# Kernel optimization log

Measured on AMD Instinct MI355X. Metric: run time of the kernel, lower is better.

## Reference

```python
import jax, jax.numpy as jnp
import numpy as np

DIM = 2048
HEADS = 16
HEAD_DIM = DIM // HEADS
EPS = 1e-5


def layernorm(x, g, b):
    mu = jnp.mean(x, axis=-1, keepdims=True)
    var = jnp.mean(jnp.square(x - mu), axis=-1, keepdims=True)
    return (x - mu) * jax.lax.rsqrt(var + EPS) * g + b


def bitlinear(x, w):
    # BitNet b1.58: per-tensor ternary weight quant + per-token int8 absmax activation quant
    ws = jnp.clip(jnp.mean(jnp.abs(w)), 1e-5, None)          # weight scale (mean |w|)
    wq = jnp.clip(jnp.round(w / ws), -1.0, 1.0) * ws          # ternary {-1,0,1}*ws
    xs = 127.0 / jnp.clip(jnp.max(jnp.abs(x), axis=-1, keepdims=True), 1e-5, None)
    xq = jnp.clip(jnp.round(x * xs), -128.0, 127.0) / xs      # int8 absmax, dequantized
    return jnp.einsum('bnc,oc->bno', xq, wq)


def attention(x, w_qkv, w_proj):
    B, N, C = x.shape
    qkv = bitlinear(x, w_qkv).reshape(B, N, 3, HEADS, HEAD_DIM)
    q, k, v = [qkv[:, :, i].transpose(0, 2, 1, 3) for i in range(3)]  # [B,H,N,D]
    scores = jnp.einsum('bhqd,bhkd->bhqk', q, k) / jnp.sqrt(jnp.asarray(HEAD_DIM, x.dtype))
    attn = jax.nn.softmax(scores, axis=-1)
    o = jnp.einsum('bhqk,bhkd->bhqd', attn, v)
    o = o.transpose(0, 2, 1, 3).reshape(B, N, C)
    return bitlinear(o, w_proj)


def setup_inputs() -> dict:
    key = jax.random.key(0)
    ks = jax.random.split(key, 9)
    s = 0.02
    return {
        'x': jax.random.normal(ks[0], (2, 2048, DIM), dtype=jnp.float32),
        'w_qkv': jax.random.normal(ks[1], (3 * DIM, DIM), dtype=jnp.float32) * s,
        'w_proj': jax.random.normal(ks[2], (DIM, DIM), dtype=jnp.float32) * s,
        'w_fc1': jax.random.normal(ks[3], (4 * DIM, DIM), dtype=jnp.float32) * s,
        'w_fc2': jax.random.normal(ks[4], (DIM, 4 * DIM), dtype=jnp.float32) * s,
        'g1': jnp.ones((DIM,), jnp.float32),
        'b1': jnp.zeros((DIM,), jnp.float32),
        'g2': jnp.ones((DIM,), jnp.float32),
        'b2': jnp.zeros((DIM,), jnp.float32),
    }


def reference(x, w_qkv, w_proj, w_fc1, w_fc2, g1, b1, g2, b2):
    x = x + attention(layernorm(x, g1, b1), w_qkv, w_proj)
    h = bitlinear(layernorm(x, g2, b2), w_fc1)
    h = jax.nn.gelu(h, approximate=False)
    h = bitlinear(h, w_fc2)
    return x + h
```

## Files before the change

### kernel.cpp

```cpp
#include <hip/hip_runtime.h>
#include <cstdint>

#define DEVI __device__ __forceinline__

typedef int v4i __attribute__((ext_vector_type(4)));
typedef short v8s __attribute__((ext_vector_type(8)));
typedef float v4f __attribute__((ext_vector_type(4)));

DEVI float bf_lo(unsigned u) { return __uint_as_float(u << 16); }
DEVI float bf_hi(unsigned u) { return __uint_as_float(u & 0xffff0000u); }
DEVI float bf2f(unsigned short h) { return __uint_as_float(((unsigned)h) << 16); }
DEVI unsigned short f2bf(float f) {
  unsigned u = __float_as_uint(f);
  u += 0x7fffu + ((u >> 16) & 1u);
  return (unsigned short)(u >> 16);
}

DEVI void async_copy16(void* l, const void* g) {
  __builtin_amdgcn_global_load_lds((const __attribute__((address_space(1))) void*)g,
                                   (__attribute__((address_space(3))) void*)l,
                                   16, 0, 0);
}

DEVI float wave_sum(float v) {
#pragma unroll
  for (int o = 32; o > 0; o >>= 1) v += __shfl_xor(v, o, 64);
  return v;
}
DEVI float wave_max(float v) {
#pragma unroll
  for (int o = 32; o > 0; o >>= 1) v = fmaxf(v, __shfl_xor(v, o, 64));
  return v;
}

__global__ __launch_bounds__(256) void absum_kernel(const float* __restrict__ w, long n,
                                                    float* __restrict__ acc) {
  long stride = (long)gridDim.x * 1024;
  float s = 0.f;
  for (long i = ((long)blockIdx.x * 256 + threadIdx.x) * 4; i < n; i += stride) {
    float4 v = *(const float4*)(w + i);
    s += fabsf(v.x) + fabsf(v.y) + fabsf(v.z) + fabsf(v.w);
  }
  s = wave_sum(s);
  __shared__ float sc[4];
  int tid = threadIdx.x;
  if ((tid & 63) == 0) sc[tid >> 6] = s;
  __syncthreads();
  if (tid == 0) atomicAdd(acc, sc[0] + sc[1] + sc[2] + sc[3]);
}

__global__ __launch_bounds__(256) void wquant_kernel(const float* __restrict__ w, long n4,
                                                     const float* __restrict__ acc, float cnt,
                                                     signed char* __restrict__ out, int kshift) {
  float wsv = fmaxf(acc[0] / cnt, 1e-5f);
  float inv = 1.0f / wsv;
  int K = 1 << kshift;
  long stride = (long)gridDim.x * 256;
  for (long i = (long)blockIdx.x * 256 + threadIdx.x; i < n4; i += stride) {
    float4 v = *(const float4*)(w + i * 4);
    int q0 = max(-1, min(1, (int)rintf(v.x * inv)));
    int q1 = max(-1, min(1, (int)rintf(v.y * inv)));
    int q2 = max(-1, min(1, (int)rintf(v.z * inv)));
    int q3 = max(-1, min(1, (int)rintf(v.w * inv)));
    unsigned r = (q0 & 0xff) | ((q1 & 0xff) << 8) | ((q2 & 0xff) << 16) | ((q3 & 0xff) << 24);
    long flat = i * 4;
    int n = (int)(flat >> kshift);
    int k = (int)(flat & (K - 1));
    long off = ((long)(n >> 4) * (K >> 6) + (k >> 6)) * 1024 +
               (((k >> 4) & 3) * 16 + (n & 15)) * 16 + (k & 15);
    *(unsigned*)(out + off) = r;
  }
}

__global__ __launch_bounds__(256) void ln_quant_kernel(const float* __restrict__ x,
                                                       const float* __restrict__ g,
                                                       const float* __restrict__ b,
                                                       signed char* __restrict__ q,
                                                       float* __restrict__ inv_s) {
  int row = blockIdx.x, tid = threadIdx.x;
  const float4* xr = (const float4*)(x + (long)row * 2048);
  float4 a0 = xr[tid * 2], a1 = xr[tid * 2 + 1];
  float xv[8] = {a0.x, a0.y, a0.z, a0.w, a1.x, a1.y, a1.z, a1.w};
  float s = 0.f, s2 = 0.f;
#pragma unroll
  for (int e = 0; e < 8; ++e) { s += xv[e]; s2 += xv[e] * xv[e]; }
  s = wave_sum(s); s2 = wave_sum(s2);
  __shared__ float sc[8];
  if ((tid & 63) == 0) { sc[tid >> 6] = s; sc[4 + (tid >> 6)] = s2; }
  __syncthreads();
  float mean = (sc[0] + sc[1] + sc[2] + sc[3]) * (1.f / 2048.f);
  float var = (sc[4] + sc[5] + sc[6] + sc[7]) * (1.f / 2048.f) - mean * mean;
  float rs = 1.0f / sqrtf(var + 1e-5f);
  float4 g0 = ((const float4*)g)[tid * 2], g1v = ((const float4*)g)[tid * 2 + 1];
  float4 b0 = ((const float4*)b)[tid * 2], b1v = ((const float4*)b)[tid * 2 + 1];
  float gv[8] = {g0.x, g0.y, g0.z, g0.w, g1v.x, g1v.y, g1v.z, g1v.w};
  float bv[8] = {b0.x, b0.y, b0.z, b0.w, b1v.x, b1v.y, b1v.z, b1v.w};
  float y[8];
  float am = 0.f;
#pragma unroll
  for (int e = 0; e < 8; ++e) {
    y[e] = (xv[e] - mean) * rs * gv[e] + bv[e];
    am = fmaxf(am, fabsf(y[e]));
  }
  am = wave_max(am);
  __syncthreads();
  if ((tid & 63) == 0) sc[tid >> 6] = am;
  __syncthreads();
  am = fmaxf(fmaxf(sc[0], sc[1]), fmaxf(sc[2], sc[3]));
  float c = fmaxf(am, 1e-5f);
  float xs = 127.0f / c;
  union { signed char c8[8]; int2 v; } u;
#pragma unroll
  for (int e = 0; e < 8; ++e) {
    int t = (int)rintf(y[e] * xs);
    u.c8[e] = (signed char)max(-128, min(127, t));
  }
  ((int2*)(q + (long)row * 2048))[tid] = u.v;
  if (tid == 0) inv_s[row] = c * (1.0f / 127.0f);
}

template <int R>
__global__ __launch_bounds__(256) void row_quant_kernel(const unsigned short* __restrict__ in,
                                                        signed char* __restrict__ q,
                                                        float* __restrict__ inv_s) {
  constexpr int V = R / 2048;
  int row = blockIdx.x, tid = threadIdx.x;
  const uint4* p = (const uint4*)(in + (long)row * R);
  float y[V * 8];
  float am = 0.f;
#pragma unroll
  for (int v = 0; v < V; ++v) {
    uint4 d = p[tid * V + v];
    unsigned xw[4] = {d.x, d.y, d.z, d.w};
#pragma unroll
    for (int k = 0; k < 4; ++k) {
      y[v * 8 + k * 2] = bf_lo(xw[k]);
      y[v * 8 + k * 2 + 1] = bf_hi(xw[k]);
    }
  }
#pragma unroll
  for (int e = 0; e < V * 8; ++e) am = fmaxf(am, fabsf(y[e]));
  am = wave_max(am);
  __shared__ float sc[4];
  if ((tid & 63) == 0) sc[tid >> 6] = am;
  __syncthreads();
  am = fmaxf(fmaxf(sc[0], sc[1]), fmaxf(sc[2], sc[3]));
  float c = fmaxf(am, 1e-5f);
  float xs = 127.0f / c;
  signed char* qr = q + (long)row * R;
#pragma unroll
  for (int v = 0; v < V; ++v) {
    union { signed char c8[8]; long l; } u;
#pragma unroll
    for (int k = 0; k < 8; ++k) {
      int t = (int)rintf(y[v * 8 + k] * xs);
      u.c8[k] = (signed char)max(-128, min(127, t));
    }
    ((long*)qr)[tid * V + v] = u.l;
  }
  if (tid == 0) inv_s[row] = c * (1.0f / 127.0f);
}

template <int EPI>
__global__ __launch_bounds__(256)
void gemm_i8(const signed char* __restrict__ A, const signed char* __restrict__ Bp,
             int N, int K, const float* __restrict__ wacc, float wcount,
             const float* __restrict__ inv_s, const float* __restrict__ res,
             void* __restrict__ outp) {
  __shared__ signed char As[2][128 * 128];
  int tid = threadIdx.x;
  int idx = blockIdx.x;
  int r8 = idx & 7, rest = idx >> 3;
  int mb = rest & 31;
  int nb = (rest >> 5) * 8 + r8;
  int m0 = mb * 128, n0 = nb * 128;
  int w = tid >> 6, lane = tid & 63;
  int wm = (w >> 1) * 64, wn = (w & 1) * 64;
  int lr = lane & 15, q = lane >> 4;

  v4i acc[4][4] = {};

  int srow = w * 32 + (lane >> 3);
  int scol = (lane & 7) ^ ((lane >> 3) & 7);
  const signed char* ga = A + (long)(m0 + srow) * K + scol * 16;

  int nkb = K >> 7;
  const signed char* gbp[4];
#pragma unroll
  for (int t = 0; t < 4; ++t) {
    int ntile = (n0 >> 4) + (w & 1) * 4 + t;
    gbp[t] = Bp + (long)ntile * (K >> 6) * 1024 + lane * 16;
  }

  v4i bf_cur[2][4], bf_nxt[2][4];
#pragma unroll
  for (int i = 0; i < 4; ++i)
    async_copy16(&As[0][(w * 256 + i * 64) * 16], ga + i * 8 * K);
#pragma unroll
  for (int s = 0; s < 2; ++s)
#pragma unroll
    for (int t = 0; t < 4; ++t) bf_cur[s][t] = *(const v4i*)(gbp[t] + s * 1024);
  __syncthreads();

  int buf = 0;
  for (int kb = 0; kb < nkb; ++kb) {
    if (kb + 1 < nkb) {
#pragma unroll
      for (int i = 0; i < 4; ++i)
        async_copy16(&As[buf ^ 1][(w * 256 + i * 64) * 16], ga + i * 8 * K + (kb + 1) * 128);
#pragma unroll
      for (int s = 0; s < 2; ++s)
#pragma unroll
        for (int t = 0; t < 4; ++t)
          bf_nxt[s][t] = *(const v4i*)(gbp[t] + ((kb + 1) * 2 + s) * 1024);
    }
#pragma unroll
    for (int s = 0; s < 2; ++s) {
      v4i af[4];
#pragma unroll
      for (int i = 0; i < 4; ++i) {
        int row = wm + i * 16 + lr;
        af[i] = *(const v4i*)(&As[buf][(row * 8 + ((s * 4 + q) ^ (lr & 7))) * 16]);
      }
#pragma unroll
      for (int i = 0; i < 4; ++i)
#pragma unroll
        for (int j = 0; j < 4; ++j)
          acc[i][j] = __builtin_amdgcn_mfma_i32_16x16x64_i8(af[i], bf_cur[s][j], acc[i][j], 0, 0, 0);
    }
    __syncthreads();
    if (kb + 1 < nkb) {
#pragma unroll
      for (int s = 0; s < 2; ++s)
#pragma unroll
        for (int t = 0; t < 4; ++t) bf_cur[s][t] = bf_nxt[s][t];
    }
    buf ^= 1;
  }

  float wsv = fmaxf(wacc[0] / wcount, 1e-5f);
#pragma unroll
  for (int i = 0; i < 4; ++i) {
    int rowbase = m0 + wm + i * 16 + (lane >> 4) * 4;
#pragma unroll
    for (int r = 0; r < 4; ++r) {
      int row = rowbase + r;
      float s = wsv * inv_s[row];
#pragma unroll
      for (int j = 0; j < 4; ++j) {
        int col = n0 + wn + j * 16 + (lane & 15);
        long off = (long)row * N + col;
        float v = (float)acc[i][j][r] * s;
        if constexpr (EPI == 0) {
          ((unsigned short*)outp)[off] = f2bf(v);
        } else if constexpr (EPI == 1) {
          ((float*)outp)[off] = v + res[off];
        } else {
          float gvv = 0.5f * v * (1.0f + erff(v * 0.70710678118654752f));
          ((unsigned short*)outp)[off] = f2bf(gvv);
        }
      }
    }
  }
}

__global__ __launch_bounds__(256, 2)
void fattn_kernel(const unsigned short* __restrict__ qkv, float* __restrict__ O0,
                  float* __restrict__ O1, float2* __restrict__ stats) {
  constexpr int VROW = 72;
  constexpr int PROW = 72;
  __shared__ char Ks[16384];
  __shared__ unsigned short Vt[128 * VROW];
  __shared__ unsigned short Ps[4 * 32 * PROW];

  int tid = threadIdx.x;
  int w = tid >> 6, lane = tid & 63;
  int l = lane & 15, q = lane >> 4;
  int idx = blockIdx.x;
  int r8 = idx & 7, rest = idx >> 3;
  int ks = rest & 1;
  int qt = (rest >> 1) & 15;
  int bh = (rest >> 5) * 8 + r8;
  int bb = bh >> 4, hh = bh & 15;
  const unsigned short* base = qkv + (long)bb * 2048 * 6144;
  int q0 = qt * 128;
  float* Opart = ks ? O1 : O0;

  v8s aq[2][4];
#pragma unroll
  for (int s = 0; s < 2; ++s) {
    const unsigned short* qrow = base + (long)(q0 + w * 32 + s * 16 + l) * 6144 + hh * 128;
#pragma unroll
    for (int kf = 0; kf < 4; ++kf) aq[s][kf] = *(const v8s*)(qrow + kf * 32 + q * 8);
  }

  v4f oacc[2][8];
#pragma unroll
  for (int s = 0; s < 2; ++s)
#pragma unroll
    for (int t = 0; t < 8; ++t) oacc[s][t] = (v4f){0.f, 0.f, 0.f, 0.f};
  float mrow[2][4], lrow[2][4];
#pragma unroll
  for (int s = 0; s < 2; ++s)
#pragma unroll
    for (int r = 0; r < 4; ++r) { mrow[s][r] = -1e30f; lrow[s][r] = 0.f; }

  unsigned short* pw = Ps + w * 32 * PROW;
  const unsigned short* kbase_g = base + 2048 + hh * 128;
  const unsigned short* vbase_g = base + 4096 + hh * 128;
  int kg = tid & 7, dg = tid >> 3;
  constexpr float SC = 0.08838834764831845f;

  for (int kt = ks * 16; kt < ks * 16 + 16; ++kt) {
    int k0 = kt * 64;
#pragma unroll
    for (int i = 0; i < 4; ++i) {
      int c = i * 256 + w * 64 + lane;
      int key = c >> 4;
      int dch = (c & 15) ^ (key & 15);
      async_copy16(Ks + (i * 256 + w * 64) * 16,
                   kbase_g + (long)(k0 + key) * 6144 + dch * 8);
    }
    {
      uint2 lv[8];
#pragma unroll
      for (int i = 0; i < 8; ++i)
        lv[i] = *(const uint2*)(vbase_g + (long)(k0 + kg * 8 + i) * 6144 + dg * 4);
#pragma unroll
      for (int jd = 0; jd < 4; ++jd) {
        v8s pk;
#pragma unroll
        for (int i = 0; i < 8; ++i) {
          unsigned word = (jd < 2) ? lv[i].x : lv[i].y;
          pk[i] = (short)((jd & 1) ? (word >> 16) : (word & 0xffffu));
        }
        *(v8s*)(Vt + (dg * 4 + jd) * VROW + kg * 8) = pk;
      }
    }
    __syncthreads();

    v4f sacc[2][4];
#pragma unroll
    for (int s = 0; s < 2; ++s)
#pragma unroll
      for (int t = 0; t < 4; ++t) sacc[s][t] = (v4f){0.f, 0.f, 0.f, 0.f};
#pragma unroll
    for (int kf = 0; kf < 4; ++kf) {
#pragma unroll
      for (int t = 0; t < 4; ++t) {
        int ch = (t * 16 + l) * 16 + ((kf * 4 + q) ^ l);
        v8s bk = *(const v8s*)(Ks + ch * 16);
        sacc[0][t] = __builtin_amdgcn_mfma_f32_16x16x32_bf16(aq[0][kf], bk, sacc[0][t], 0, 0, 0);
        sacc[1][t] = __builtin_amdgcn_mfma_f32_16x16x32_bf16(aq[1][kf], bk, sacc[1][t], 0, 0, 0);
      }
    }
#pragma unroll
    for (int s = 0; s < 2; ++s) {
      float rmax[4], alpha[4], rsum[4];
#pragma unroll
      for (int r = 0; r < 4; ++r) {
        rmax[r] = fmaxf(fmaxf(sacc[s][0][r], sacc[s][1][r]),
                        fmaxf(sacc[s][2][r], sacc[s][3][r])) * SC;
#pragma unroll
        for (int msk = 1; msk < 16; msk <<= 1) rmax[r] = fmaxf(rmax[r], __shfl_xor(rmax[r], msk, 64));
        float mnew = fmaxf(mrow[s][r], rmax[r]);
        alpha[r] = __expf(mrow[s][r] - mnew);
        mrow[s][r] = mnew;
        rsum[r] = 0.f;
      }
#pragma unroll
      for (int t = 0; t < 4; ++t) {
#pragma unroll
        for (int r = 0; r < 4; ++r) {
          float p = __expf(sacc[s][t][r] * SC - mrow[s][r]);
          rsum[r] += p;
          pw[(s * 16 + q * 4 + r) * PROW + t * 16 + l] = f2bf(p);
        }
      }
#pragma unroll
      for (int r = 0; r < 4; ++r) {
#pragma unroll
        for (int msk = 1; msk < 16; msk <<= 1) rsum[r] += __shfl_xor(rsum[r], msk, 64);
        lrow[s][r] = lrow[s][r] * alpha[r] + rsum[r];
#pragma unroll
        for (int t = 0; t < 8; ++t) oacc[s][t][r] *= alpha[r];
      }
    }
#pragma unroll
    for (int s2 = 0; s2 < 2; ++s2) {
      v8s ap0 = *(const v8s*)(pw + l * PROW + s2 * 32 + q * 8);
      v8s ap1 = *(const v8s*)(pw + (16 + l) * PROW + s2 * 32 + q * 8);
#pragma unroll
      for (int t = 0; t < 8; ++t) {
        v8s bv = *(const v8s*)(Vt + (t * 16 + l) * VROW + s2 * 32 + q * 8);
        oacc[0][t] = __builtin_amdgcn_mfma_f32_16x16x32_bf16(ap0, bv, oacc[0][t], 0, 0, 0);
        oacc[1][t] = __builtin_amdgcn_mfma_f32_16x16x32_bf16(ap1, bv, oacc[1][t], 0, 0, 0);
      }
    }
    __syncthreads();
  }

#pragma unroll
  for (int s = 0; s < 2; ++s) {
#pragma unroll
    for (int t = 0; t < 8; ++t) {
#pragma unroll
      for (int r = 0; r < 4; ++r) {
        long grow = bb * 2048 + q0 + w * 32 + s * 16 + q * 4 + r;
        Opart[grow * 2048 + hh * 128 + t * 16 + l] = oacc[s][t][r];
      }
    }
    if (l == 0) {
#pragma unroll
      for (int r = 0; r < 4; ++r) {
        long grow = bb * 2048 + q0 + w * 32 + s * 16 + q * 4 + r;
        stats[((long)ks * 4096 + grow) * 16 + hh] = make_float2(mrow[s][r], lrow[s][r]);
      }
    }
  }
}

__global__ __launch_bounds__(256)
void attn_combine(const float* __restrict__ O0, const float* __restrict__ O1,
                  const float2* __restrict__ stats, unsigned short* __restrict__ o) {
  int grow = blockIdx.x, tid = threadIdx.x;
  int hh = tid >> 4;
  float2 s0 = stats[(long)grow * 16 + hh];
  float2 s1 = stats[((long)4096 + grow) * 16 + hh];
  float m = fmaxf(s0.x, s1.x);
  float e0 = __expf(s0.x - m), e1 = __expf(s1.x - m);
  float inv = 1.0f / (s0.y * e0 + s1.y * e1);
  long base = (long)grow * 2048 + tid * 8;
  float4 a0 = *(const float4*)(O0 + base), a1 = *(const float4*)(O0 + base + 4);
  float4 c0 = *(const float4*)(O1 + base), c1 = *(const float4*)(O1 + base + 4);
  unsigned short r[8];
  r[0] = f2bf((a0.x * e0 + c0.x * e1) * inv);
  r[1] = f2bf((a0.y * e0 + c0.y * e1) * inv);
  r[2] = f2bf((a0.z * e0 + c0.z * e1) * inv);
  r[3] = f2bf((a0.w * e0 + c0.w * e1) * inv);
  r[4] = f2bf((a1.x * e0 + c1.x * e1) * inv);
  r[5] = f2bf((a1.y * e0 + c1.y * e1) * inv);
  r[6] = f2bf((a1.z * e0 + c1.z * e1) * inv);
  r[7] = f2bf((a1.w * e0 + c1.w * e1) * inv);
  *(uint4*)(o + base) = *(uint4*)r;
}

extern "C" void kernel_launch(void* const* d_in, const int* in_sizes, int n_in,
                              void* d_out, int out_size, void* d_ws, size_t ws_size,
                              hipStream_t stream) {
  (void)in_sizes; (void)n_in; (void)out_size; (void)ws_size;
  const float* x      = (const float*)d_in[0];
  const float* w_qkv  = (const float*)d_in[1];
  const float* w_proj = (const float*)d_in[2];
  const float* w_fc1  = (const float*)d_in[3];
  const float* w_fc2  = (const float*)d_in[4];
  const float* g1 = (const float*)d_in[5];
  const float* b1 = (const float*)d_in[6];
  const float* g2 = (const float*)d_in[7];
  const float* b2 = (const float*)d_in[8];

  char* wsb = (char*)d_ws;
  float* acc = (float*)wsb;
  size_t off = 256;
  signed char* q8 = (signed char*)(wsb + off);       off += (size_t)4096 * 8192;
  float* invs = (float*)(wsb + off);                 off += 16384;
  signed char* wq_qkv = (signed char*)(wsb + off);   off += (size_t)6144 * 2048;
  signed char* wq_proj = (signed char*)(wsb + off);  off += (size_t)2048 * 2048;
  signed char* wq_fc1 = (signed char*)(wsb + off);   off += (size_t)8192 * 2048;
  signed char* wq_fc2 = (signed char*)(wsb + off);   off += (size_t)2048 * 8192;
  unsigned short* qkvh = (unsigned short*)(wsb + off); off += (size_t)4096 * 8192 * 2;
  unsigned short* obuf = (unsigned short*)(wsb + off); off += (size_t)4096 * 2048 * 2;
  float* x2 = (float*)(wsb + off);                   off += (size_t)4096 * 2048 * 4;
  float2* stats = (float2*)(wsb + off);              off += (size_t)2 * 4096 * 16 * 8;
  float* O0 = x2;
  float* O1 = (float*)q8;

  hipMemsetAsync(acc, 0, 256, stream);

  absum_kernel<<<dim3(1024), 256, 0, stream>>>(w_qkv, (long)6144 * 2048, acc + 0);
  absum_kernel<<<dim3(512),  256, 0, stream>>>(w_proj, (long)2048 * 2048, acc + 1);
  absum_kernel<<<dim3(1024), 256, 0, stream>>>(w_fc1, (long)8192 * 2048, acc + 2);
  absum_kernel<<<dim3(1024), 256, 0, stream>>>(w_fc2, (long)2048 * 8192, acc + 3);

  wquant_kernel<<<dim3(1024), 256, 0, stream>>>(w_qkv, (long)6144 * 2048 / 4, acc + 0, 12582912.f, wq_qkv, 11);
  wquant_kernel<<<dim3(1024), 256, 0, stream>>>(w_proj, (long)2048 * 2048 / 4, acc + 1, 4194304.f, wq_proj, 11);
  wquant_kernel<<<dim3(1024), 256, 0, stream>>>(w_fc1, (long)8192 * 2048 / 4, acc + 2, 16777216.f, wq_fc1, 11);
  wquant_kernel<<<dim3(1024), 256, 0, stream>>>(w_fc2, (long)2048 * 8192 / 4, acc + 3, 16777216.f, wq_fc2, 13);

  ln_quant_kernel<<<4096, 256, 0, stream>>>(x, g1, b1, q8, invs);
  gemm_i8<0><<<48 * 32, 256, 0, stream>>>(q8, wq_qkv, 6144, 2048, acc + 0, 12582912.f, invs, nullptr, qkvh);
  fattn_kernel<<<1024, 256, 0, stream>>>(qkvh, O0, O1, stats);
  attn_combine<<<4096, 256, 0, stream>>>(O0, O1, stats, obuf);
  row_quant_kernel<2048><<<4096, 256, 0, stream>>>(obuf, q8, invs);
  gemm_i8<1><<<16 * 32, 256, 0, stream>>>(q8, wq_proj, 2048, 2048, acc + 1, 4194304.f, invs, x, x2);
  ln_quant_kernel<<<4096, 256, 0, stream>>>(x2, g2, b2, q8, invs);
  gemm_i8<2><<<64 * 32, 256, 0, stream>>>(q8, wq_fc1, 8192, 2048, acc + 2, 16777216.f, invs, nullptr, qkvh);
  row_quant_kernel<8192><<<4096, 256, 0, stream>>>(qkvh, q8, invs);
  gemm_i8<1><<<16 * 32, 256, 0, stream>>>(q8, wq_fc2, 2048, 8192, acc + 3, 16777216.f, invs, x2, (float*)d_out);
}
```

Baseline: 851.4 us.

## Rewrite flash attention with double-buffered K/V, register P, no split-K combine

Flash attention is restructured: K/V tiles are double-buffered in shared memory so the next tile loads while the current one computes. S is computed transposed so P stays in registers, packed with v_cvt_pk_bf16 and fed straight into the PV MFMA without an LDS round trip. The rescale is lazy, skipped unless the max grows by more than 8. The two-way key split and its separate combine kernel are removed, and each block now processes all 32 key tiles with 512 threads. This saves the fp32 partial-output traffic and a launch, but halves the number of blocks and lengthens each block's serial loop.

```diff
diff --git a/kernel.cpp b/kernel.cpp
--- a/kernel.cpp
+++ b/kernel.cpp
@@ -264,185 +264,167 @@
   }
 }
 
-__global__ __launch_bounds__(256, 2)
-void fattn_kernel(const unsigned short* __restrict__ qkv, float* __restrict__ O0,
-                  float* __restrict__ O1, float2* __restrict__ stats) {
+
+DEVI int sigma_k(int y) {
+  return (y & 35) | (((y >> 3) & 1) << 4) | (((y >> 2) & 1) << 3) | (((y >> 4) & 1) << 2);
+}
+
+DEVI void stage_k(const unsigned short* kbase_g, int k0, char* ks, int w, int lane) {
+#pragma unroll
+  for (int i = 0; i < 2; ++i) {
+    int c = i * 512 + w * 64 + lane;
+    int key = c >> 4;
+    int dch = (c & 15) ^ (key & 15);
+    async_copy16(ks + (i * 512 + w * 64) * 16,
+                 kbase_g + (long)(k0 + sigma_k(key)) * 6144 + dch * 8);
+  }
+}
+
+DEVI void load_v(const unsigned short* vbase_g, int k0, int kg, int dg, uint2* lv) {
+#pragma unroll
+  for (int i = 0; i < 4; ++i)
+    lv[i] = *(const uint2*)(vbase_g + (long)(k0 + kg * 4 + i) * 6144 + dg * 4);
+}
+
+DEVI void repack_v(const uint2* lv, unsigned short* vt, int kg, int dg) {
+#pragma unroll
+  for (int jd = 0; jd < 4; ++jd) {
+    union { unsigned short s[4]; unsigned long long u; } pk;
+#pragma unroll
+    for (int i = 0; i < 4; ++i) {
+      unsigned word = (jd < 2) ? lv[i].x : lv[i].y;
+      pk.s[i] = (unsigned short)((jd & 1) ? (word >> 16) : (word & 0xffffu));
+    }
+    *(unsigned long long*)(vt + (dg * 4 + jd) * 72 + kg * 4) = pk.u;
+  }
+}
+
+__global__ __launch_bounds__(512, 4)
+void fattn_kernel(const unsigned short* __restrict__ qkv, unsigned short* __restrict__ out) {
   constexpr int VROW = 72;
-  constexpr int PROW = 72;
-  __shared__ char Ks[16384];
-  __shared__ unsigned short Vt[128 * VROW];
-  __shared__ unsigned short Ps[4 * 32 * PROW];
+  __shared__ __align__(16) char Ks[2][16384];
+  __shared__ __align__(16) unsigned short Vt[2][128 * VROW];
 
   int tid = threadIdx.x;
   int w = tid >> 6, lane = tid & 63;
   int l = lane & 15, q = lane >> 4;
   int idx = blockIdx.x;
   int r8 = idx & 7, rest = idx >> 3;
-  int ks = rest & 1;
-  int qt = (rest >> 1) & 15;
-  int bh = (rest >> 5) * 8 + r8;
+  int qt = rest & 15;
+  int bh = (rest >> 4) * 8 + r8;
   int bb = bh >> 4, hh = bh & 15;
   const unsigned short* base = qkv + (long)bb * 2048 * 6144;
   int q0 = qt * 128;
-  float* Opart = ks ? O1 : O0;
-
-  v8s aq[2][4];
-#pragma unroll
-  for (int s = 0; s < 2; ++s) {
-    const unsigned short* qrow = base + (long)(q0 + w * 32 + s * 16 + l) * 6144 + hh * 128;
-#pragma unroll
-    for (int kf = 0; kf < 4; ++kf) aq[s][kf] = *(const v8s*)(qrow + kf * 32 + q * 8);
-  }
-
-  v4f oacc[2][8];
-#pragma unroll
-  for (int s = 0; s < 2; ++s)
-#pragma unroll
-    for (int t = 0; t < 8; ++t) oacc[s][t] = (v4f){0.f, 0.f, 0.f, 0.f};
-  float mrow[2][4], lrow[2][4];
-#pragma unroll
-  for (int s = 0; s < 2; ++s)
-#pragma unroll
-    for (int r = 0; r < 4; ++r) { mrow[s][r] = -1e30f; lrow[s][r] = 0.f; }
-
-  unsigned short* pw = Ps + w * 32 * PROW;
+
+  v8s aq[4];
+  {
+    const unsigned short* qrow = base + (long)(q0 + w * 16 + l) * 6144 + hh * 128;
+#pragma unroll
+    for (int kf = 0; kf < 4; ++kf) aq[kf] = *(const v8s*)(qrow + kf * 32 + q * 8);
+  }
+
+  v4f oacc[8] = {};
+  float mrow = -1e30f, lrow = 0.f;
+
   const unsigned short* kbase_g = base + 2048 + hh * 128;
   const unsigned short* vbase_g = base + 4096 + hh * 128;
-  int kg = tid & 7, dg = tid >> 3;
+  int kg = tid & 15, dg = tid >> 4;
   constexpr float SC = 0.08838834764831845f;
 
-  for (int kt = ks * 16; kt < ks * 16 + 16; ++kt) {
-    int k0 = kt * 64;
-#pragma unroll
-    for (int i = 0; i < 4; ++i) {
-      int c = i * 256 + w * 64 + lane;
-      int key = c >> 4;
-      int dch = (c & 15) ^ (key & 15);
-      async_copy16(Ks + (i * 256 + w * 64) * 16,
-                   kbase_g + (long)(k0 + key) * 6144 + dch * 8);
-    }
-    {
-      uint2 lv[8];
-#pragma unroll
-      for (int i = 0; i < 8; ++i)
-        lv[i] = *(const uint2*)(vbase_g + (long)(k0 + kg * 8 + i) * 6144 + dg * 4);
-#pragma unroll
-      for (int jd = 0; jd < 4; ++jd) {
-        v8s pk;
-#pragma unroll
-        for (int i = 0; i < 8; ++i) {
-          unsigned word = (jd < 2) ? lv[i].x : lv[i].y;
-          pk[i] = (short)((jd & 1) ? (word >> 16) : (word & 0xffffu));
-        }
-        *(v8s*)(Vt + (dg * 4 + jd) * VROW + kg * 8) = pk;
-      }
-    }
-    __syncthreads();
-
-    v4f sacc[2][4];
-#pragma unroll
-    for (int s = 0; s < 2; ++s)
-#pragma unroll
-      for (int t = 0; t < 4; ++t) sacc[s][t] = (v4f){0.f, 0.f, 0.f, 0.f};
+  stage_k(kbase_g, 0, Ks[0], w, lane);
+  uint2 lv[4];
+  load_v(vbase_g, 0, kg, dg, lv);
+  repack_v(lv, Vt[0], kg, dg);
+  __syncthreads();
+
+  for (int kt = 0; kt < 32; ++kt) {
+    const char* ksc = Ks[kt & 1];
+    const unsigned short* vtc = Vt[kt & 1];
+    bool more = kt < 31;
+    if (more) {
+      stage_k(kbase_g, (kt + 1) * 64, Ks[(kt + 1) & 1], w, lane);
+      load_v(vbase_g, (kt + 1) * 64, kg, dg, lv);
+    }
+
+    v4f sacc[4] = {};
 #pragma unroll
     for (int kf = 0; kf < 4; ++kf) {
 #pragma unroll
       for (int t = 0; t < 4; ++t) {
         int ch = (t * 16 + l) * 16 + ((kf * 4 + q) ^ l);
-        v8s bk = *(const v8s*)(Ks + ch * 16);
-        sacc[0][t] = __builtin_amdgcn_mfma_f32_16x16x32_bf16(aq[0][kf], bk, sacc[0][t], 0, 0, 0);
-        sacc[1][t] = __builtin_amdgcn_mfma_f32_16x16x32_bf16(aq[1][kf], bk, sacc[1][t], 0, 0, 0);
-      }
-    }
-#pragma unroll
-    for (int s = 0; s < 2; ++s) {
-      float rmax[4], alpha[4], rsum[4];
+        v8s bk = *(const v8s*)(ksc + ch * 16);
+        sacc[t] = __builtin_amdgcn_mfma_f32_16x16x32_bf16(bk, aq[kf], sacc[t], 0, 0, 0);
+      }
+    }
+
+    float rm = -1e30f;
+#pragma unroll
+    for (int t = 0; t < 4; ++t)
+#pragma unroll
+      for (int r = 0; r < 4; ++r) rm = fmaxf(rm, sacc[t][r]);
+    rm *= SC;
+    rm = fmaxf(rm, __shfl_xor(rm, 16, 64));
+    rm = fmaxf(rm, __shfl_xor(rm, 32, 64));
+    float mnew = fmaxf(mrow, rm);
+    if (__any(mnew - mrow > 8.0f)) {
+      float alpha = __expf(mrow - mnew);
+      mrow = mnew;
+      lrow *= alpha;
 #pragma unroll
       for (int r = 0; r < 4; ++r) {
-        rmax[r] = fmaxf(fmaxf(sacc[s][0][r], sacc[s][1][r]),
-                        fmaxf(sacc[s][2][r], sacc[s][3][r])) * SC;
-#pragma unroll
-        for (int msk = 1; msk < 16; msk <<= 1) rmax[r] = fmaxf(rmax[r], __shfl_xor(rmax[r], msk, 64));
-        float mnew = fmaxf(mrow[s][r], rmax[r]);
-        alpha[r] = __expf(mrow[s][r] - mnew);
-        mrow[s][r] = mnew;
-        rsum[r] = 0.f;
-      }
-#pragma unroll
-      for (int t = 0; t < 4; ++t) {
-#pragma unroll
-        for (int r = 0; r < 4; ++r) {
-          float p = __expf(sacc[s][t][r] * SC - mrow[s][r]);
-          rsum[r] += p;
-          pw[(s * 16 + q * 4 + r) * PROW + t * 16 + l] = f2bf(p);
-        }
-      }
+        float ao = __shfl(alpha, q * 4 + r, 64);
+#pragma unroll
+        for (int t = 0; t < 8; ++t) oacc[t][r] *= ao;
+      }
+    }
+    float rs = 0.f;
+#pragma unroll
+    for (int t = 0; t < 4; ++t)
 #pragma unroll
       for (int r = 0; r < 4; ++r) {
-#pragma unroll
-        for (int msk = 1; msk < 16; msk <<= 1) rsum[r] += __shfl_xor(rsum[r], msk, 64);
-        lrow[s][r] = lrow[s][r] * alpha[r] + rsum[r];
-#pragma unroll
-        for (int t = 0; t < 8; ++t) oacc[s][t][r] *= alpha[r];
-      }
-    }
+        float pv = __expf(fmaf(sacc[t][r], SC, -mrow));
+        sacc[t][r] = pv;
+        rs += pv;
+      }
+    rs += __shfl_xor(rs, 16, 64);
+    rs += __shfl_xor(rs, 32, 64);
+    lrow += rs;
+
+    union { unsigned u[4]; v8s s; } pa[2];
+#pragma unroll
+    for (int s2 = 0; s2 < 2; ++s2)
+#pragma unroll
+      for (int j2 = 0; j2 < 4; ++j2) {
+        int tt = s2 * 2 + (j2 >> 1);
+        int r0 = (j2 & 1) * 2;
+        unsigned wrd;
+        asm("v_cvt_pk_bf16_f32 %0, %1, %2"
+            : "=v"(wrd) : "v"(sacc[tt][r0]), "v"(sacc[tt][r0 + 1]));
+        pa[s2].u[j2] = wrd;
+      }
+
 #pragma unroll
     for (int s2 = 0; s2 < 2; ++s2) {
-      v8s ap0 = *(const v8s*)(pw + l * PROW + s2 * 32 + q * 8);
-      v8s ap1 = *(const v8s*)(pw + (16 + l) * PROW + s2 * 32 + q * 8);
 #pragma unroll
       for (int t = 0; t < 8; ++t) {
-        v8s bv = *(const v8s*)(Vt + (t * 16 + l) * VROW + s2 * 32 + q * 8);
-        oacc[0][t] = __builtin_amdgcn_mfma_f32_16x16x32_bf16(ap0, bv, oacc[0][t], 0, 0, 0);
-        oacc[1][t] = __builtin_amdgcn_mfma_f32_16x16x32_bf16(ap1, bv, oacc[1][t], 0, 0, 0);
-      }
-    }
+        v8s bv = *(const v8s*)(vtc + (t * 16 + l) * VROW + s2 * 32 + q * 8);
+        oacc[t] = __builtin_amdgcn_mfma_f32_16x16x32_bf16(pa[s2].s, bv, oacc[t], 0, 0, 0);
+      }
+    }
+
+    if (more) repack_v(lv, Vt[(kt + 1) & 1], kg, dg);
     __syncthreads();
   }
 
 #pragma unroll
-  for (int s = 0; s < 2; ++s) {
-#pragma unroll
-    for (int t = 0; t < 8; ++t) {
-#pragma unroll
-      for (int r = 0; r < 4; ++r) {
-        long grow = bb * 2048 + q0 + w * 32 + s * 16 + q * 4 + r;
-        Opart[grow * 2048 + hh * 128 + t * 16 + l] = oacc[s][t][r];
-      }
-    }
-    if (l == 0) {
-#pragma unroll
-      for (int r = 0; r < 4; ++r) {
-        long grow = bb * 2048 + q0 + w * 32 + s * 16 + q * 4 + r;
-        stats[((long)ks * 4096 + grow) * 16 + hh] = make_float2(mrow[s][r], lrow[s][r]);
-      }
-    }
-  }
-}
-
-__global__ __launch_bounds__(256)
-void attn_combine(const float* __restrict__ O0, const float* __restrict__ O1,
-                  const float2* __restrict__ stats, unsigned short* __restrict__ o) {
-  int grow = blockIdx.x, tid = threadIdx.x;
-  int hh = tid >> 4;
-  float2 s0 = stats[(long)grow * 16 + hh];
-  float2 s1 = stats[((long)4096 + grow) * 16 + hh];
-  float m = fmaxf(s0.x, s1.x);
-  float e0 = __expf(s0.x - m), e1 = __expf(s1.x - m);
-  float inv = 1.0f / (s0.y * e0 + s1.y * e1);
-  long base = (long)grow * 2048 + tid * 8;
-  float4 a0 = *(const float4*)(O0 + base), a1 = *(const float4*)(O0 + base + 4);
-  float4 c0 = *(const float4*)(O1 + base), c1 = *(const float4*)(O1 + base + 4);
-  unsigned short r[8];
-  r[0] = f2bf((a0.x * e0 + c0.x * e1) * inv);
-  r[1] = f2bf((a0.y * e0 + c0.y * e1) * inv);
-  r[2] = f2bf((a0.z * e0 + c0.z * e1) * inv);
-  r[3] = f2bf((a0.w * e0 + c0.w * e1) * inv);
-  r[4] = f2bf((a1.x * e0 + c1.x * e1) * inv);
-  r[5] = f2bf((a1.y * e0 + c1.y * e1) * inv);
-  r[6] = f2bf((a1.z * e0 + c1.z * e1) * inv);
-  r[7] = f2bf((a1.w * e0 + c1.w * e1) * inv);
-  *(uint4*)(o + base) = *(uint4*)r;
+  for (int r = 0; r < 4; ++r) {
+    float lr = __shfl(lrow, q * 4 + r, 64);
+    float inv = 1.0f / lr;
+    long grow = (long)bb * 2048 + q0 + w * 16 + q * 4 + r;
+    unsigned short* orow = out + grow * 2048 + hh * 128;
+#pragma unroll
+    for (int t = 0; t < 8; ++t) orow[t * 16 + l] = f2bf(oacc[t][r] * inv);
+  }
 }
 
 extern "C" void kernel_launch(void* const* d_in, const int* in_sizes, int n_in,
@@ -471,9 +453,6 @@
   unsigned short* qkvh = (unsigned short*)(wsb + off); off += (size_t)4096 * 8192 * 2;
   unsigned short* obuf = (unsigned short*)(wsb + off); off += (size_t)4096 * 2048 * 2;
   float* x2 = (float*)(wsb + off);                   off += (size_t)4096 * 2048 * 4;
-  float2* stats = (float2*)(wsb + off);              off += (size_t)2 * 4096 * 16 * 8;
-  float* O0 = x2;
-  float* O1 = (float*)q8;
 
   hipMemsetAsync(acc, 0, 256, stream);
 
@@ -489,8 +468,7 @@
 
   ln_quant_kernel<<<4096, 256, 0, stream>>>(x, g1, b1, q8, invs);
   gemm_i8<0><<<48 * 32, 256, 0, stream>>>(q8, wq_qkv, 6144, 2048, acc + 0, 12582912.f, invs, nullptr, qkvh);
-  fattn_kernel<<<1024, 256, 0, stream>>>(qkvh, O0, O1, stats);
-  attn_combine<<<4096, 256, 0, stream>>>(O0, O1, stats, obuf);
+  fattn_kernel<<<512, 512, 0, stream>>>(qkvh, obuf);
   row_quant_kernel<2048><<<4096, 256, 0, stream>>>(obuf, q8, invs);
   gemm_i8<1><<<16 * 32, 256, 0, stream>>>(q8, wq_proj, 2048, 2048, acc + 1, 4194304.f, invs, x, x2);
   ln_quant_kernel<<<4096, 256, 0, stream>>>(x2, g2, b2, q8, invs);
```

After: 761.1 us. 1.12x faster.
